# Performance work log

Measured on AMD Instinct MI355X. Metric: run time of the kernel, lower is better.

## Reference

```python
import jax, jax.numpy as jnp
import numpy as np

BS, NQ, DIM, HEADS, POINTS, LEVELS = 2, 4096, 768, 6, 4, 1
HD = DIM // HEADS
H = W = 64
NV = H * W
EPS = 1e-6


def setup_inputs() -> dict:
    key = jax.random.key(0)
    ks = jax.random.split(key, 16)
    s = 0.02  # param init scale
    return {
        "query": jax.random.normal(ks[0], (BS, NQ, DIM), jnp.float32),
        "reference_points": jax.random.uniform(ks[1], (BS, NQ, LEVELS, 2), jnp.float32),
        "feat": jax.random.normal(ks[2], (BS, NV, DIM), jnp.float32),
        "spatial_shapes": np.array([[H, W]], dtype=np.int64),
        "level_start_index": np.array([0], dtype=np.int64),
        "ln_w": jnp.ones((DIM,), jnp.float32),
        "ln_b": jnp.zeros((DIM,), jnp.float32),
        "vp_w": jax.random.normal(ks[3], (DIM, DIM), jnp.float32) * s,
        "vp_b": jnp.zeros((DIM,), jnp.float32),
        "off_w": jax.random.normal(ks[4], (DIM, HEADS * LEVELS * POINTS * 2), jnp.float32) * s,
        "off_b": jax.random.normal(ks[5], (HEADS * LEVELS * POINTS * 2,), jnp.float32),
        "aw_w": jax.random.normal(ks[6], (DIM, HEADS * LEVELS * POINTS), jnp.float32) * s,
        "aw_b": jnp.zeros((HEADS * LEVELS * POINTS,), jnp.float32),
        "out_w": jax.random.normal(ks[7], (DIM, DIM), jnp.float32) * s,
        "out_b": jnp.zeros((DIM,), jnp.float32),
        "gamma": jax.random.normal(ks[8], (DIM,), jnp.float32) * 0.1,
    }


def _layernorm(x, w, b):
    mu = jnp.mean(x, axis=-1, keepdims=True)
    var = jnp.mean(jnp.square(x - mu), axis=-1, keepdims=True)
    return (x - mu) * jax.lax.rsqrt(var + EPS) * w + b


def _bilinear_sample(img, loc):
    # img: (bs, heads, H, W, hd); loc: (bs, nq, heads, points, 2) in [0,1]
    # matches torch.grid_sample(align_corners=False, padding_mode='zeros')
    bs, heads, h, w, hd = img.shape
    x = loc[..., 0] * w - 0.5
    y = loc[..., 1] * h - 0.5
    x0 = jnp.floor(x)
    y0 = jnp.floor(y)
    wx = x - x0
    wy = y - y0
    x0i = x0.astype(jnp.int32)
    y0i = y0.astype(jnp.int32)
    bi = jnp.arange(bs)[:, None, None, None]
    hi = jnp.arange(heads)[None, None, :, None]

    def gather(yi, xi):
        valid = (xi >= 0) & (xi < w) & (yi >= 0) & (yi < h)
        v = img[bi, hi, jnp.clip(yi, 0, h - 1), jnp.clip(xi, 0, w - 1)]
        return v * valid[..., None].astype(img.dtype)

    v00 = gather(y0i, x0i)
    v01 = gather(y0i, x0i + 1)
    v10 = gather(y0i + 1, x0i)
    v11 = gather(y0i + 1, x0i + 1)
    wx = wx[..., None]
    wy = wy[..., None]
    return (v00 * (1 - wy) * (1 - wx) + v01 * (1 - wy) * wx
            + v10 * wy * (1 - wx) + v11 * wy * wx)


def _msda(q, value, reference_points, spatial_shapes, off_w, off_b, aw_w, aw_b, out_w, out_b):
    bs, nq, _ = q.shape
    nv = value.shape[1]
    value = value.reshape(bs, nv, HEADS, HD)
    offsets = (q @ off_w + off_b).reshape(bs, nq, HEADS, LEVELS, POINTS, 2)
    aw = jax.nn.softmax(q @ aw_w + aw_b, axis=-1).reshape(bs, nq, HEADS, LEVELS, POINTS)
    # offset_normalizer = [W_l, H_l] per level
    norm = jnp.asarray(np.asarray(spatial_shapes)[:, ::-1], jnp.float32)  # (L, 2)
    loc = reference_points[:, :, None, :, None, :] + offsets / norm[None, None, None, :, None, :]
    # loc: (bs, nq, heads, levels, points, 2)
    out = jnp.zeros((bs, nq, HEADS, HD), jnp.float32)
    start = 0
    for l in range(LEVELS):
        h_l, w_l = int(spatial_shapes[l][0]), int(spatial_shapes[l][1])
        img = value[:, start:start + h_l * w_l].reshape(bs, h_l, w_l, HEADS, HD).transpose(0, 3, 1, 2, 4)
        sampled = _bilinear_sample(img, loc[:, :, :, l])  # (bs, nq, heads, points, hd)
        out = out + jnp.einsum('bnhpd,bnhp->bnhd', sampled, aw[:, :, :, l])
        start += h_l * w_l
    return out.reshape(bs, nq, DIM) @ out_w + out_b


def reference(query, reference_points, feat, spatial_shapes, level_start_index,
              ln_w, ln_b, vp_w, vp_b, off_w, off_b, aw_w, aw_b, out_w, out_b, gamma):
    q = _layernorm(query, ln_w, ln_b)
    value = feat @ vp_w + vp_b
    attn = _msda(q, value, reference_points, spatial_shapes,
                 off_w, off_b, aw_w, aw_b, out_w, out_b)
    # identity = zeros, dropout = 0 -> attn as-is; residual scale by gamma
    return query + gamma * attn
```

## Files before the change

### kernel.cpp

```cpp
#include <hip/hip_runtime.h>
#include <hip/hip_bf16.h>
#include <math.h>

#define BSZ 2
#define NQ 4096
#define DIM 768
#define HEADS 6
#define POINTS 4
#define HD 128
#define HW_DIM 64
#define NV (HW_DIM*HW_DIM)
#define M_TOTAL (BSZ*NQ)
#define KDIM 768

#define BM 64
#define BN 128
#define BKK 64
#define NBLK_M (M_TOTAL/BM)
#define NBLK_N (DIM/BN)
#define GEMM_GRID (NBLK_M*NBLK_N)
#define CVT_BLOCKS (M_TOTAL/4)
#define TR_BLOCKS (576+576+72)
#define SMALL_BLOCKS (M_TOTAL/64)

typedef __attribute__((ext_vector_type(8))) short bf16x8;
typedef __attribute__((ext_vector_type(4))) float f32x4;
typedef unsigned int u32;
typedef unsigned short u16;

__device__ inline u16 f2bf(float f) {
    union { float f; u32 u; } v; v.f = f;
    u32 r = v.u + 0x7fffu + ((v.u >> 16) & 1u);
    return (u16)(r >> 16);
}

#define GLD16(g, l) __builtin_amdgcn_global_load_lds( \
    (const __attribute__((address_space(1))) u32*)(g), \
    (__attribute__((address_space(3))) u32*)(l), 16, 0, 0)

__global__ __launch_bounds__(256) void prep_kernel(
        const float* __restrict__ feat, u16* __restrict__ feat_bf,
        const float* __restrict__ vp_w,  u16* __restrict__ vp_wt,
        const float* __restrict__ out_w, u16* __restrict__ out_wt,
        const float* __restrict__ off_w, const float* __restrict__ aw_w,
        u16* __restrict__ oaw_wt) {
    int b = blockIdx.x;
    if (b < CVT_BLOCKS) {
        int wave = threadIdx.x >> 6, lane = threadIdx.x & 63;
        int row = b * 4 + wave;
        int c = lane * 4;
        const float* fr = feat + (size_t)row * DIM;
        float4 f0 = *(const float4*)(fr + c);
        float4 f1 = *(const float4*)(fr + c + 256);
        float4 f2 = *(const float4*)(fr + c + 512);
        u16* fb = feat_bf + (size_t)row * DIM;
        ushort4 fo;
        fo.x = f2bf(f0.x); fo.y = f2bf(f0.y); fo.z = f2bf(f0.z); fo.w = f2bf(f0.w);
        *(ushort4*)(fb + c) = fo;
        fo.x = f2bf(f1.x); fo.y = f2bf(f1.y); fo.z = f2bf(f1.z); fo.w = f2bf(f1.w);
        *(ushort4*)(fb + c + 256) = fo;
        fo.x = f2bf(f2.x); fo.y = f2bf(f2.y); fo.z = f2bf(f2.z); fo.w = f2bf(f2.w);
        *(ushort4*)(fb + c + 512) = fo;
    } else {
        int t = b - CVT_BLOCKS;
        int z, xk, yk;
        if (t < 576)      { z = 0; xk = t % 24; yk = t / 24; }
        else if (t < 1152){ z = 1; t -= 576; xk = t % 24; yk = t / 24; }
        else              { z = 2; t -= 1152; xk = t % 3; yk = t / 3; }
        __shared__ float tile[32][33];
        int n0 = xk * 32, k0 = yk * 32;
        int tx = threadIdx.x & 31, ty = threadIdx.x >> 5;
        const float* src = (z == 0) ? vp_w : (z == 1) ? out_w : nullptr;
        u16* dst = (z == 0) ? vp_wt : (z == 1) ? out_wt : oaw_wt;
        #pragma unroll
        for (int r = 0; r < 4; r++) {
            int k = k0 + ty + r * 8, n = n0 + tx;
            float v = 0.0f;
            if (z < 2) {
                v = src[(size_t)k * DIM + n];
            } else {
                if (n < 48) v = off_w[(size_t)k * 48 + n];
                else if (n < 72) v = aw_w[(size_t)k * 24 + (n - 48)];
            }
            tile[ty + r * 8][tx] = v;
        }
        __syncthreads();
        #pragma unroll
        for (int r = 0; r < 4; r++) {
            int nn = ty + r * 8, kk = tx;
            int drow = n0 + nn;
            if (z == 2 && drow >= 80) continue;
            dst[(size_t)drow * KDIM + k0 + kk] = f2bf(tile[kk][nn]);
        }
    }
}

__device__ __forceinline__ void gemm_big_body(int b,
        const u16* __restrict__ A, const u16* __restrict__ Bt,
        const float* __restrict__ bias, void* __restrict__ Cout,
        int storeBF16, const float* __restrict__ resid,
        const float* __restrict__ gamma) {
    __shared__ u16 As[BM * BKK];
    __shared__ u16 Bs[BN * BKK];
    int tid = threadIdx.x, w = tid >> 6, lane = tid & 63;
    int lm = lane & 15, quad = lane >> 4;
    int xcd = b & 7, idx = b >> 3;
    int mb = xcd * 16 + idx / NBLK_N;
    int nb = idx % NBLK_N;
    int m0 = mb * BM, n0 = nb * BN;
    int wr = w & 1, wc = w >> 1;

    int srow = lane >> 3;
    int scol = (lane & 7) ^ srow;
    const u16* Ab = A + (size_t)m0 * KDIM;
    const u16* Bb = Bt + (size_t)n0 * KDIM;

    f32x4 acc[2][4];
    #pragma unroll
    for (int i = 0; i < 2; i++)
        #pragma unroll
        for (int j = 0; j < 4; j++) acc[i][j] = (f32x4){0.f, 0.f, 0.f, 0.f};

    const u16* aaddr[2][2];
    const u16* baddr[4][2];
    #pragma unroll
    for (int i = 0; i < 2; i++) {
        int row = wr * 32 + i * 16 + lm;
        #pragma unroll
        for (int kk = 0; kk < 2; kk++)
            aaddr[i][kk] = &As[row * BKK + (((quad + 4 * kk) ^ (row & 7)) << 3)];
    }
    #pragma unroll
    for (int j = 0; j < 4; j++) {
        int row = wc * 64 + j * 16 + lm;
        #pragma unroll
        for (int kk = 0; kk < 2; kk++)
            baddr[j][kk] = &Bs[row * BKK + (((quad + 4 * kk) ^ (row & 7)) << 3)];
    }

    for (int k0 = 0; k0 < KDIM; k0 += BKK) {
        #pragma unroll
        for (int r = 0; r < 2; r++) {
            int row = r * 32 + w * 8 + srow;
            GLD16(Ab + (size_t)row * KDIM + k0 + scol * 8, &As[(r * 32 + w * 8) * BKK]);
        }
        #pragma unroll
        for (int r = 0; r < 4; r++) {
            int row = r * 32 + w * 8 + srow;
            GLD16(Bb + (size_t)row * KDIM + k0 + scol * 8, &Bs[(r * 32 + w * 8) * BKK]);
        }
        __syncthreads();
        #pragma unroll
        for (int kk = 0; kk < 2; kk++) {
            bf16x8 af[2], bf[4];
            #pragma unroll
            for (int i = 0; i < 2; i++) af[i] = *(const bf16x8*)aaddr[i][kk];
            #pragma unroll
            for (int j = 0; j < 4; j++) bf[j] = *(const bf16x8*)baddr[j][kk];
            #pragma unroll
            for (int i = 0; i < 2; i++)
                #pragma unroll
                for (int j = 0; j < 4; j++)
                    acc[i][j] = __builtin_amdgcn_mfma_f32_16x16x32_bf16(af[i], bf[j], acc[i][j], 0, 0, 0);
        }
        __syncthreads();
    }

    #pragma unroll
    for (int j = 0; j < 4; j++) {
        int col = n0 + wc * 64 + j * 16 + lm;
        float bb = bias[col];
        #pragma unroll
        for (int i = 0; i < 2; i++) {
            #pragma unroll
            for (int r = 0; r < 4; r++) {
                int row = m0 + wr * 32 + i * 16 + quad * 4 + r;
                size_t idxo = (size_t)row * DIM + col;
                float v = acc[i][j][r] + bb;
                if (storeBF16) {
                    ((u16*)Cout)[idxo] = f2bf(v);
                } else {
                    ((float*)Cout)[idxo] = resid[idxo] + gamma[col] * v;
                }
            }
        }
    }
}

__device__ __forceinline__ void gemm_small_body(int mblk,
        const float* __restrict__ query, const float* __restrict__ lnw,
        const float* __restrict__ lnb, const u16* __restrict__ Bt,
        const float* __restrict__ b0, const float* __restrict__ b1,
        float* __restrict__ C) {
    __shared__ u16 As2[64 * 32];
    __shared__ u16 Bs2[80 * 32];
    __shared__ float s_mu[64], s_rs[64];
    int tid = threadIdx.x, wave = tid >> 6, lane = tid & 63;
    int lm = lane & 15, quad = lane >> 4;
    int m0 = mblk * 64;

    #pragma unroll 4
    for (int it = 0; it < 16; it++) {
        int row = it * 4 + wave;
        const float* xr = query + (size_t)(m0 + row) * DIM + lane * 4;
        float4 v0 = *(const float4*)(xr);
        float4 v1 = *(const float4*)(xr + 256);
        float4 v2 = *(const float4*)(xr + 512);
        float s  = v0.x+v0.y+v0.z+v0.w + v1.x+v1.y+v1.z+v1.w + v2.x+v2.y+v2.z+v2.w;
        float ss = v0.x*v0.x+v0.y*v0.y+v0.z*v0.z+v0.w*v0.w
                 + v1.x*v1.x+v1.y*v1.y+v1.z*v1.z+v1.w*v1.w
                 + v2.x*v2.x+v2.y*v2.y+v2.z*v2.z+v2.w*v2.w;
        #pragma unroll
        for (int st = 1; st < 64; st <<= 1) {
            s  += __shfl_xor(s,  st, 64);
            ss += __shfl_xor(ss, st, 64);
        }
        if (lane == 0) {
            float mean = s * (1.0f / DIM);
            float var  = ss * (1.0f / DIM) - mean * mean;
            s_mu[row] = mean;
            s_rs[row] = rsqrtf(var + 1e-6f);
        }
    }
    __syncthreads();

    f32x4 acc[5];
    #pragma unroll
    for (int i = 0; i < 5; i++) acc[i] = (f32x4){0.f, 0.f, 0.f, 0.f};
    int arow = tid >> 2;
    int acol = (tid & 3) * 8;
    int lrow = lane >> 2, lcol = (lane & 3) * 8;

    for (int k0 = 0; k0 < KDIM; k0 += 32) {
        {
            const float* xr = query + (size_t)(m0 + arow) * DIM + k0 + acol;
            float4 a = *(const float4*)xr;
            float4 b = *(const float4*)(xr + 4);
            float4 w0 = *(const float4*)(lnw + k0 + acol);
            float4 w1 = *(const float4*)(lnw + k0 + acol + 4);
            float4 c0 = *(const float4*)(lnb + k0 + acol);
            float4 c1 = *(const float4*)(lnb + k0 + acol + 4);
            float mu = s_mu[arow], rs = s_rs[arow];
            ushort4 o0, o1;
            o0.x = f2bf((a.x - mu) * rs * w0.x + c0.x);
            o0.y = f2bf((a.y - mu) * rs * w0.y + c0.y);
            o0.z = f2bf((a.z - mu) * rs * w0.z + c0.z);
            o0.w = f2bf((a.w - mu) * rs * w0.w + c0.w);
            o1.x = f2bf((b.x - mu) * rs * w1.x + c1.x);
            o1.y = f2bf((b.y - mu) * rs * w1.y + c1.y);
            o1.z = f2bf((b.z - mu) * rs * w1.z + c1.z);
            o1.w = f2bf((b.w - mu) * rs * w1.w + c1.w);
            *(ushort4*)&As2[arow * 32 + acol]     = o0;
            *(ushort4*)&As2[arow * 32 + acol + 4] = o1;
        }
        for (int c = wave; c < 5; c += 4) {
            GLD16(Bt + (size_t)(c * 16 + lrow) * KDIM + k0 + lcol, &Bs2[c * 16 * 32]);
        }
        __syncthreads();
        bf16x8 af = *(const bf16x8*)&As2[(wave * 16 + lm) * 32 + quad * 8];
        #pragma unroll
        for (int bn = 0; bn < 5; bn++) {
            bf16x8 bv = *(const bf16x8*)&Bs2[(bn * 16 + lm) * 32 + quad * 8];
            acc[bn] = __builtin_amdgcn_mfma_f32_16x16x32_bf16(af, bv, acc[bn], 0, 0, 0);
        }
        __syncthreads();
    }
    #pragma unroll
    for (int bn = 0; bn < 5; bn++) {
        int col = bn * 16 + lm;
        float bb = (col < 48) ? b0[col] : ((col < 72) ? b1[col - 48] : 0.0f);
        #pragma unroll
        for (int r = 0; r < 4; r++) {
            int row = m0 + wave * 16 + quad * 4 + r;
            C[(size_t)row * 80 + col] = acc[bn][r] + bb;
        }
    }
}

__global__ __launch_bounds__(256, 4) void gemms_kernel(
        const u16* __restrict__ feat_bf, const u16* __restrict__ vp_wt,
        const float* __restrict__ vp_b, u16* __restrict__ v_bf,
        const float* __restrict__ query, const float* __restrict__ lnw,
        const float* __restrict__ lnb, const u16* __restrict__ oaw_wt,
        const float* __restrict__ off_b, const float* __restrict__ aw_b,
        float* __restrict__ oa) {
    int b = blockIdx.x;
    if (b < GEMM_GRID) {
        gemm_big_body(b, feat_bf, vp_wt, vp_b, v_bf, 1, nullptr, nullptr);
    } else {
        gemm_small_body(b - GEMM_GRID, query, lnw, lnb, oaw_wt, off_b, aw_b, oa);
    }
}

__global__ __launch_bounds__(256, 4) void outgemm_kernel(
        const u16* __restrict__ s_bf, const u16* __restrict__ out_wt,
        const float* __restrict__ out_b, float* __restrict__ out_f,
        const float* __restrict__ query, const float* __restrict__ gamma) {
    gemm_big_body(blockIdx.x, s_bf, out_wt, out_b, out_f, 0, query, gamma);
}

__global__ __launch_bounds__(192) void sample_kernel(
        const float* __restrict__ oa, const float* __restrict__ refp,
        const u16* __restrict__ v, u16* __restrict__ out) {
    int row = blockIdx.x;
    int b = row >> 12;
    int tid = threadIdx.x;
    __shared__ float s_w[4][24];
    __shared__ int   s_o[4][24];
    __shared__ float s_e[24];
    if (tid < 24) {
        int h = tid >> 2, p = tid & 3;
        const float* pp = oa + (size_t)row * 80;
        float ox = pp[h * 8 + p * 2 + 0];
        float oy = pp[h * 8 + p * 2 + 1];
        float lg = pp[48 + tid];
        float rx = refp[row * 2 + 0], ry = refp[row * 2 + 1];
        float x = (rx + ox * (1.0f / HW_DIM)) * HW_DIM - 0.5f;
        float y = (ry + oy * (1.0f / HW_DIM)) * HW_DIM - 0.5f;
        float fx = floorf(x), fy = floorf(y);
        int x0 = (int)fx, y0 = (int)fy;
        int x1 = x0 + 1, y1 = y0 + 1;
        float wx = x - fx, wy = y - fy;
        float vx0 = (x0 >= 0 && x0 < HW_DIM) ? 1.f : 0.f;
        float vx1 = (x1 >= 0 && x1 < HW_DIM) ? 1.f : 0.f;
        float vy0 = (y0 >= 0 && y0 < HW_DIM) ? 1.f : 0.f;
        float vy1 = (y1 >= 0 && y1 < HW_DIM) ? 1.f : 0.f;
        int xc0 = min(max(x0, 0), HW_DIM - 1), xc1 = min(max(x1, 0), HW_DIM - 1);
        int yc0 = min(max(y0, 0), HW_DIM - 1), yc1 = min(max(y1, 0), HW_DIM - 1);
        int base = b * NV * DIM;
        s_o[0][tid] = base + (yc0 * HW_DIM + xc0) * DIM;
        s_o[1][tid] = base + (yc0 * HW_DIM + xc1) * DIM;
        s_o[2][tid] = base + (yc1 * HW_DIM + xc0) * DIM;
        s_o[3][tid] = base + (yc1 * HW_DIM + xc1) * DIM;
        s_w[0][tid] = (1.f - wy) * (1.f - wx) * vy0 * vx0;
        s_w[1][tid] = (1.f - wy) * wx * vy0 * vx1;
        s_w[2][tid] = wy * (1.f - wx) * vy1 * vx0;
        s_w[3][tid] = wy * wx * vy1 * vx1;
        s_e[tid] = lg;
        float m = s_e[0];
        #pragma unroll
        for (int i = 1; i < 24; i++) m = fmaxf(m, s_e[i]);
        s_e[tid] = expf(lg - m);
    }
    __syncthreads();
    float ssum = 0.0f;
    #pragma unroll
    for (int i = 0; i < 24; i++) ssum += s_e[i];
    float inv = 1.0f / ssum;

    int h = tid >> 5;
    int d4 = (tid & 31) * 4;
    const u16* vb = v + h * HD + d4;
    float a0 = 0.f, a1 = 0.f, a2 = 0.f, a3 = 0.f;
    #pragma unroll
    for (int p = 0; p < 4; p++) {
        int idx = h * 4 + p;
        float aw = s_e[idx] * inv;
        #pragma unroll
        for (int c = 0; c < 4; c++) {
            uint2 u = *(const uint2*)(vb + s_o[c][idx]);
            float w = aw * s_w[c][idx];
            a0 += w * __uint_as_float(u.x << 16);
            a1 += w * __uint_as_float(u.x & 0xffff0000u);
            a2 += w * __uint_as_float(u.y << 16);
            a3 += w * __uint_as_float(u.y & 0xffff0000u);
        }
    }
    uint2 pack;
    pack.x = (u32)f2bf(a0) | ((u32)f2bf(a1) << 16);
    pack.y = (u32)f2bf(a2) | ((u32)f2bf(a3) << 16);
    *(uint2*)&out[(size_t)row * DIM + h * HD + d4] = pack;
}

extern "C" void kernel_launch(void* const* d_in, const int* in_sizes, int n_in,
                              void* d_out, int out_size, void* d_ws, size_t ws_size,
                              hipStream_t stream) {
    const float* query = (const float*)d_in[0];
    const float* refp  = (const float*)d_in[1];
    const float* feat  = (const float*)d_in[2];
    const float* ln_w  = (const float*)d_in[5];
    const float* ln_b  = (const float*)d_in[6];
    const float* vp_w  = (const float*)d_in[7];
    const float* vp_b  = (const float*)d_in[8];
    const float* off_w = (const float*)d_in[9];
    const float* off_b = (const float*)d_in[10];
    const float* aw_w  = (const float*)d_in[11];
    const float* aw_b  = (const float*)d_in[12];
    const float* out_w = (const float*)d_in[13];
    const float* out_b = (const float*)d_in[14];
    const float* gamma = (const float*)d_in[15];

    const size_t MD = (size_t)M_TOTAL * DIM;
    char* ws = (char*)d_ws;
    u16* feat_bf = (u16*)ws;                 ws += MD * 2;
    u16* v_bf    = (u16*)ws;                 ws += MD * 2;
    u16* s_bf    = (u16*)ws;                 ws += MD * 2;
    u16* vp_wt   = (u16*)ws;                 ws += (size_t)DIM * DIM * 2;
    u16* out_wt  = (u16*)ws;                 ws += (size_t)DIM * DIM * 2;
    u16* oaw_wt  = (u16*)ws;                 ws += (size_t)80 * KDIM * 2;
    float* oa    = (float*)ws;               ws += (size_t)M_TOTAL * 80 * 4;
    float* out_f = (float*)d_out;

    prep_kernel<<<CVT_BLOCKS + TR_BLOCKS, 256, 0, stream>>>(
        feat, feat_bf, vp_w, vp_wt, out_w, out_wt, off_w, aw_w, oaw_wt);
    gemms_kernel<<<GEMM_GRID + SMALL_BLOCKS, 256, 0, stream>>>(
        feat_bf, vp_wt, vp_b, v_bf, query, ln_w, ln_b, oaw_wt, off_b, aw_b, oa);
    sample_kernel<<<M_TOTAL, 192, 0, stream>>>(oa, refp, v_bf, s_bf);
    outgemm_kernel<<<GEMM_GRID, 256, 0, stream>>>(s_bf, out_wt, out_b, out_f, query, gamma);
}
```

Before: 196.8 us.

## Fuse feat bf16 conversion into value GEMM and double-buffer GEMM tiles

The value-projection GEMM now reads fp32 feat directly, converts it to bf16 in registers and writes it into swizzled LDS, so the separate conversion pass and its bf16 workspace buffer are gone. Both big GEMMs double-buffer their LDS tiles, issuing the next tile's loads before the current MFMA work. The small LayerNorm GEMM blocks are moved to the front of the grid, and occupancy hints drop from 4 to 3 blocks to make room for the larger shared memory. The cost is more fp32 global traffic and more register pressure inside the GEMM.

```diff
diff --git a/kernel.cpp b/kernel.cpp
--- a/kernel.cpp
+++ b/kernel.cpp
@@ -19,9 +19,12 @@
 #define NBLK_M (M_TOTAL/BM)
 #define NBLK_N (DIM/BN)
 #define GEMM_GRID (NBLK_M*NBLK_N)
-#define CVT_BLOCKS (M_TOTAL/4)
 #define TR_BLOCKS (576+576+72)
-#define SMALL_BLOCKS (M_TOTAL/64)
+#define SMALL_BLOCKS 128
+
+#define A_TILE (BM*BKK)
+#define B_TILE (BN*BKK)
+#define SMEM_U16 (2*(A_TILE+B_TILE))
 
 typedef __attribute__((ext_vector_type(8))) short bf16x8;
 typedef __attribute__((ext_vector_type(4))) float f32x4;
@@ -34,74 +37,60 @@
     return (u16)(r >> 16);
 }
 
+__device__ inline u32 pkbf2(float a, float b) {
+    __hip_bfloat162 h = __float22bfloat162_rn(make_float2(a, b));
+    union { __hip_bfloat162 h; u32 u; } cv; cv.h = h; return cv.u;
+}
+
 #define GLD16(g, l) __builtin_amdgcn_global_load_lds( \
     (const __attribute__((address_space(1))) u32*)(g), \
     (__attribute__((address_space(3))) u32*)(l), 16, 0, 0)
 
-__global__ __launch_bounds__(256) void prep_kernel(
-        const float* __restrict__ feat, u16* __restrict__ feat_bf,
+__global__ __launch_bounds__(256) void tr_kernel(
         const float* __restrict__ vp_w,  u16* __restrict__ vp_wt,
         const float* __restrict__ out_w, u16* __restrict__ out_wt,
         const float* __restrict__ off_w, const float* __restrict__ aw_w,
         u16* __restrict__ oaw_wt) {
-    int b = blockIdx.x;
-    if (b < CVT_BLOCKS) {
-        int wave = threadIdx.x >> 6, lane = threadIdx.x & 63;
-        int row = b * 4 + wave;
-        int c = lane * 4;
-        const float* fr = feat + (size_t)row * DIM;
-        float4 f0 = *(const float4*)(fr + c);
-        float4 f1 = *(const float4*)(fr + c + 256);
-        float4 f2 = *(const float4*)(fr + c + 512);
-        u16* fb = feat_bf + (size_t)row * DIM;
-        ushort4 fo;
-        fo.x = f2bf(f0.x); fo.y = f2bf(f0.y); fo.z = f2bf(f0.z); fo.w = f2bf(f0.w);
-        *(ushort4*)(fb + c) = fo;
-        fo.x = f2bf(f1.x); fo.y = f2bf(f1.y); fo.z = f2bf(f1.z); fo.w = f2bf(f1.w);
-        *(ushort4*)(fb + c + 256) = fo;
-        fo.x = f2bf(f2.x); fo.y = f2bf(f2.y); fo.z = f2bf(f2.z); fo.w = f2bf(f2.w);
-        *(ushort4*)(fb + c + 512) = fo;
-    } else {
-        int t = b - CVT_BLOCKS;
-        int z, xk, yk;
-        if (t < 576)      { z = 0; xk = t % 24; yk = t / 24; }
-        else if (t < 1152){ z = 1; t -= 576; xk = t % 24; yk = t / 24; }
-        else              { z = 2; t -= 1152; xk = t % 3; yk = t / 3; }
-        __shared__ float tile[32][33];
-        int n0 = xk * 32, k0 = yk * 32;
-        int tx = threadIdx.x & 31, ty = threadIdx.x >> 5;
-        const float* src = (z == 0) ? vp_w : (z == 1) ? out_w : nullptr;
-        u16* dst = (z == 0) ? vp_wt : (z == 1) ? out_wt : oaw_wt;
-        #pragma unroll
-        for (int r = 0; r < 4; r++) {
-            int k = k0 + ty + r * 8, n = n0 + tx;
-            float v = 0.0f;
-            if (z < 2) {
-                v = src[(size_t)k * DIM + n];
-            } else {
-                if (n < 48) v = off_w[(size_t)k * 48 + n];
-                else if (n < 72) v = aw_w[(size_t)k * 24 + (n - 48)];
-            }
-            tile[ty + r * 8][tx] = v;
-        }
-        __syncthreads();
-        #pragma unroll
-        for (int r = 0; r < 4; r++) {
-            int nn = ty + r * 8, kk = tx;
-            int drow = n0 + nn;
-            if (z == 2 && drow >= 80) continue;
-            dst[(size_t)drow * KDIM + k0 + kk] = f2bf(tile[kk][nn]);
-        }
-    }
-}
-
-__device__ __forceinline__ void gemm_big_body(int b,
-        const u16* __restrict__ A, const u16* __restrict__ Bt,
+    int t = blockIdx.x;
+    int z, xk, yk;
+    if (t < 576)      { z = 0; xk = t % 24; yk = t / 24; }
+    else if (t < 1152){ z = 1; t -= 576; xk = t % 24; yk = t / 24; }
+    else              { z = 2; t -= 1152; xk = t % 3; yk = t / 3; }
+    __shared__ float tile[32][33];
+    int n0 = xk * 32, k0 = yk * 32;
+    int tx = threadIdx.x & 31, ty = threadIdx.x >> 5;
+    const float* src = (z == 0) ? vp_w : (z == 1) ? out_w : nullptr;
+    u16* dst = (z == 0) ? vp_wt : (z == 1) ? out_wt : oaw_wt;
+    #pragma unroll
+    for (int r = 0; r < 4; r++) {
+        int k = k0 + ty + r * 8, n = n0 + tx;
+        float v = 0.0f;
+        if (z < 2) {
+            v = src[(size_t)k * DIM + n];
+        } else {
+            if (n < 48) v = off_w[(size_t)k * 48 + n];
+            else if (n < 72) v = aw_w[(size_t)k * 24 + (n - 48)];
+        }
+        tile[ty + r * 8][tx] = v;
+    }
+    __syncthreads();
+    #pragma unroll
+    for (int r = 0; r < 4; r++) {
+        int nn = ty + r * 8, kk = tx;
+        int drow = n0 + nn;
+        if (z == 2 && drow >= 80) continue;
+        dst[(size_t)drow * KDIM + k0 + kk] = f2bf(tile[kk][nn]);
+    }
+}
+
+template<int AF32>
+__device__ __forceinline__ void gemm_big_body(int b, u16* __restrict__ smem,
+        const void* __restrict__ Asrc, const u16* __restrict__ Bt,
         const float* __restrict__ bias, void* __restrict__ Cout,
         int storeBF16, const float* __restrict__ resid,
         const float* __restrict__ gamma) {
-    __shared__ u16 As[BM * BKK];
-    __shared__ u16 Bs[BN * BKK];
+    u16* As = smem;
+    u16* Bs = smem + 2 * A_TILE;
     int tid = threadIdx.x, w = tid >> 6, lane = tid & 63;
     int lm = lane & 15, quad = lane >> 4;
     int xcd = b & 7, idx = b >> 3;
@@ -112,57 +101,97 @@
 
     int srow = lane >> 3;
     int scol = (lane & 7) ^ srow;
-    const u16* Ab = A + (size_t)m0 * KDIM;
+    const u16* Ab = (const u16*)Asrc + (size_t)m0 * KDIM;
+    const float* Af = (const float*)Asrc + (size_t)m0 * KDIM;
     const u16* Bb = Bt + (size_t)n0 * KDIM;
 
+    int arow0 = w * 16 + (lane >> 3);
+    int ac8   = lane & 7;
+    int aswz  = ((ac8 ^ (arow0 & 7)) << 3);
+
     f32x4 acc[2][4];
     #pragma unroll
     for (int i = 0; i < 2; i++)
         #pragma unroll
         for (int j = 0; j < 4; j++) acc[i][j] = (f32x4){0.f, 0.f, 0.f, 0.f};
 
-    const u16* aaddr[2][2];
-    const u16* baddr[4][2];
+    int aoff[2][2], boff[4][2];
     #pragma unroll
     for (int i = 0; i < 2; i++) {
         int row = wr * 32 + i * 16 + lm;
         #pragma unroll
         for (int kk = 0; kk < 2; kk++)
-            aaddr[i][kk] = &As[row * BKK + (((quad + 4 * kk) ^ (row & 7)) << 3)];
+            aoff[i][kk] = row * BKK + (((quad + 4 * kk) ^ (row & 7)) << 3);
     }
     #pragma unroll
     for (int j = 0; j < 4; j++) {
         int row = wc * 64 + j * 16 + lm;
         #pragma unroll
         for (int kk = 0; kk < 2; kk++)
-            baddr[j][kk] = &Bs[row * BKK + (((quad + 4 * kk) ^ (row & 7)) << 3)];
-    }
-
-    for (int k0 = 0; k0 < KDIM; k0 += BKK) {
+            boff[j][kk] = row * BKK + (((quad + 4 * kk) ^ (row & 7)) << 3);
+    }
+
+    auto stageB = [&](int buf, int k0) {
+        #pragma unroll
+        for (int r = 0; r < 4; r++) {
+            int row = r * 32 + w * 8 + srow;
+            GLD16(Bb + (size_t)row * KDIM + k0 + scol * 8,
+                  Bs + buf * B_TILE + (r * 32 + w * 8) * BKK);
+        }
+    };
+    auto stageA_lds = [&](int buf, int k0) {
         #pragma unroll
         for (int r = 0; r < 2; r++) {
             int row = r * 32 + w * 8 + srow;
-            GLD16(Ab + (size_t)row * KDIM + k0 + scol * 8, &As[(r * 32 + w * 8) * BKK]);
-        }
-        #pragma unroll
-        for (int r = 0; r < 4; r++) {
-            int row = r * 32 + w * 8 + srow;
-            GLD16(Bb + (size_t)row * KDIM + k0 + scol * 8, &Bs[(r * 32 + w * 8) * BKK]);
-        }
-        __syncthreads();
+            GLD16(Ab + (size_t)row * KDIM + k0 + scol * 8,
+                  As + buf * A_TILE + (r * 32 + w * 8) * BKK);
+        }
+    };
+
+    float4 l0, h0, l1, h1;
+    auto loadA_f32 = [&](int k0) {
+        const float* p0 = Af + (size_t)arow0 * KDIM + k0 + ac8 * 8;
+        const float* p1 = p0 + 8 * KDIM;
+        l0 = *(const float4*)p0; h0 = *(const float4*)(p0 + 4);
+        l1 = *(const float4*)p1; h1 = *(const float4*)(p1 + 4);
+    };
+    auto writeA_f32 = [&](int buf) {
+        uint4 pk;
+        pk.x = pkbf2(l0.x, l0.y); pk.y = pkbf2(l0.z, l0.w);
+        pk.z = pkbf2(h0.x, h0.y); pk.w = pkbf2(h0.z, h0.w);
+        *(uint4*)(As + buf * A_TILE + arow0 * BKK + aswz) = pk;
+        pk.x = pkbf2(l1.x, l1.y); pk.y = pkbf2(l1.z, l1.w);
+        pk.z = pkbf2(h1.x, h1.y); pk.w = pkbf2(h1.z, h1.w);
+        *(uint4*)(As + buf * A_TILE + (arow0 + 8) * BKK + aswz) = pk;
+    };
+
+    if (AF32) { loadA_f32(0); stageB(0, 0); writeA_f32(0); }
+    else      { stageA_lds(0, 0); stageB(0, 0); }
+    __syncthreads();
+
+    const int NT = KDIM / BKK;
+    for (int t = 0; t < NT; t++) {
+        if (t + 1 < NT) {
+            if (AF32) loadA_f32((t + 1) * BKK);
+            else      stageA_lds((t + 1) & 1, (t + 1) * BKK);
+            stageB((t + 1) & 1, (t + 1) * BKK);
+        }
+        const u16* Ap = As + (t & 1) * A_TILE;
+        const u16* Bp = Bs + (t & 1) * B_TILE;
         #pragma unroll
         for (int kk = 0; kk < 2; kk++) {
             bf16x8 af[2], bf[4];
             #pragma unroll
-            for (int i = 0; i < 2; i++) af[i] = *(const bf16x8*)aaddr[i][kk];
+            for (int i = 0; i < 2; i++) af[i] = *(const bf16x8*)(Ap + aoff[i][kk]);
             #pragma unroll
-            for (int j = 0; j < 4; j++) bf[j] = *(const bf16x8*)baddr[j][kk];
+            for (int j = 0; j < 4; j++) bf[j] = *(const bf16x8*)(Bp + boff[j][kk]);
             #pragma unroll
             for (int i = 0; i < 2; i++)
                 #pragma unroll
                 for (int j = 0; j < 4; j++)
                     acc[i][j] = __builtin_amdgcn_mfma_f32_16x16x32_bf16(af[i], bf[j], acc[i][j], 0, 0, 0);
         }
+        if (AF32 && t + 1 < NT) writeA_f32((t + 1) & 1);
         __syncthreads();
     }
 
@@ -187,14 +216,15 @@
     }
 }
 
-__device__ __forceinline__ void gemm_small_body(int mblk,
+__device__ __forceinline__ void gemm_small_body(int mblk, u16* __restrict__ smem,
         const float* __restrict__ query, const float* __restrict__ lnw,
         const float* __restrict__ lnb, const u16* __restrict__ Bt,
         const float* __restrict__ b0, const float* __restrict__ b1,
         float* __restrict__ C) {
-    __shared__ u16 As2[64 * 32];
-    __shared__ u16 Bs2[80 * 32];
-    __shared__ float s_mu[64], s_rs[64];
+    u16* As2 = smem;
+    u16* Bs2 = smem + 64 * 32;
+    float* s_mu = (float*)(smem + 64 * 32 + 80 * 32);
+    float* s_rs = s_mu + 64;
     int tid = threadIdx.x, wave = tid >> 6, lane = tid & 63;
     int lm = lane & 15, quad = lane >> 4;
     int m0 = mblk * 64;
@@ -277,26 +307,29 @@
     }
 }
 
-__global__ __launch_bounds__(256, 4) void gemms_kernel(
-        const u16* __restrict__ feat_bf, const u16* __restrict__ vp_wt,
+__global__ __launch_bounds__(256, 3) void gemms_kernel(
+        const float* __restrict__ feat, const u16* __restrict__ vp_wt,
         const float* __restrict__ vp_b, u16* __restrict__ v_bf,
         const float* __restrict__ query, const float* __restrict__ lnw,
         const float* __restrict__ lnb, const u16* __restrict__ oaw_wt,
         const float* __restrict__ off_b, const float* __restrict__ aw_b,
         float* __restrict__ oa) {
+    __shared__ __align__(16) u16 smem[SMEM_U16];
     int b = blockIdx.x;
-    if (b < GEMM_GRID) {
-        gemm_big_body(b, feat_bf, vp_wt, vp_b, v_bf, 1, nullptr, nullptr);
+    if (b < SMALL_BLOCKS) {
+        gemm_small_body(b, smem, query, lnw, lnb, oaw_wt, off_b, aw_b, oa);
     } else {
-        gemm_small_body(b - GEMM_GRID, query, lnw, lnb, oaw_wt, off_b, aw_b, oa);
-    }
-}
-
-__global__ __launch_bounds__(256, 4) void outgemm_kernel(
+        gemm_big_body<1>(b - SMALL_BLOCKS, smem, feat, vp_wt, vp_b, v_bf, 1,
+                         nullptr, nullptr);
+    }
+}
+
+__global__ __launch_bounds__(256, 3) void outgemm_kernel(
         const u16* __restrict__ s_bf, const u16* __restrict__ out_wt,
         const float* __restrict__ out_b, float* __restrict__ out_f,
         const float* __restrict__ query, const float* __restrict__ gamma) {
-    gemm_big_body(blockIdx.x, s_bf, out_wt, out_b, out_f, 0, query, gamma);
+    __shared__ __align__(16) u16 smem[SMEM_U16];
+    gemm_big_body<0>(blockIdx.x, smem, s_bf, out_wt, out_b, out_f, 0, query, gamma);
 }
 
 __global__ __launch_bounds__(192) void sample_kernel(
@@ -392,7 +425,6 @@
 
     const size_t MD = (size_t)M_TOTAL * DIM;
     char* ws = (char*)d_ws;
-    u16* feat_bf = (u16*)ws;                 ws += MD * 2;
     u16* v_bf    = (u16*)ws;                 ws += MD * 2;
     u16* s_bf    = (u16*)ws;                 ws += MD * 2;
     u16* vp_wt   = (u16*)ws;                 ws += (size_t)DIM * DIM * 2;
@@ -401,10 +433,10 @@
     float* oa    = (float*)ws;               ws += (size_t)M_TOTAL * 80 * 4;
     float* out_f = (float*)d_out;
 
-    prep_kernel<<<CVT_BLOCKS + TR_BLOCKS, 256, 0, stream>>>(
-        feat, feat_bf, vp_w, vp_wt, out_w, out_wt, off_w, aw_w, oaw_wt);
-    gemms_kernel<<<GEMM_GRID + SMALL_BLOCKS, 256, 0, stream>>>(
-        feat_bf, vp_wt, vp_b, v_bf, query, ln_w, ln_b, oaw_wt, off_b, aw_b, oa);
+    tr_kernel<<<TR_BLOCKS, 256, 0, stream>>>(
+        vp_w, vp_wt, out_w, out_wt, off_w, aw_w, oaw_wt);
+    gemms_kernel<<<SMALL_BLOCKS + GEMM_GRID, 256, 0, stream>>>(
+        feat, vp_wt, vp_b, v_bf, query, ln_w, ln_b, oaw_wt, off_b, aw_b, oa);
     sample_kernel<<<M_TOTAL, 192, 0, stream>>>(oa, refp, v_bf, s_bf);
     outgemm_kernel<<<GEMM_GRID, 256, 0, stream>>>(s_bf, out_wt, out_b, out_f, query, gamma);
 }
```

Measured after the change: 191.4 us. -2.8%, faster.
